# Optimization experiments

Hardware: AMD Instinct MI355X
Metric: run time of the kernel (lower is better)

The kernel has to match this reference:

```python
import jax, jax.numpy as jnp
import numpy as np

BETA = 0.9
ADAPT_RATE = 0.1


def _surrogate_spike(x):
    gate = jax.nn.sigmoid(5.0 * x)
    hard = (x > 0).astype(x.dtype)
    return jax.lax.stop_gradient(hard - gate) + gate


def setup_inputs() -> dict:
    key = jax.random.key(0)
    k1, k2, k3, k4, k5 = jax.random.split(key, 5)
    B, T, D, H = 64, 256, 512, 1024
    x = jax.random.normal(k1, (B, T, D), dtype=jnp.float32)
    # fc_in: Linear(D, H); fc_out: Linear(H, 1)
    W_in = jax.random.normal(k2, (H, D), dtype=jnp.float32) * (1.0 / np.sqrt(D))
    b_in = jax.random.normal(k3, (H,), dtype=jnp.float32) * 0.01
    W_out = jax.random.normal(k4, (1, H), dtype=jnp.float32) * (1.0 / np.sqrt(H))
    b_out = jax.random.normal(k5, (1,), dtype=jnp.float32) * 0.01
    return {"x": x, "W_in": W_in, "b_in": b_in, "W_out": W_out, "b_out": b_out}


def reference(x, W_in, b_in, W_out, b_out):
    B, T, D = x.shape
    H = W_in.shape[0]
    # batch fc_in over all timesteps outside the recurrence
    pre = jnp.einsum('btd,hd->bth', x, W_in) + b_in  # [B,T,H]

    def step(carry, p_t):
        mem, adapt = carry
        mem = BETA * mem + p_t - adapt
        spk = _surrogate_spike(mem)
        adapt = adapt + ADAPT_RATE * spk
        mem = mem - spk  # reset_mode == 'subtract'
        return (mem, adapt), spk

    init = (jnp.zeros((B, H), x.dtype), jnp.zeros((B, H), x.dtype))
    _, spks = jax.lax.scan(step, init, jnp.swapaxes(pre, 0, 1))  # spks: [T,B,H]

    # mean_t fc_out(spk_t) == fc_out(mean_t spk_t) since fc_out is affine
    spk_mean = spks.mean(axis=0)  # [B,H]
    return spk_mean @ W_out.T + b_out  # [B,1]
```

## Files before the change

kernel.cpp:

```cpp
#include <hip/hip_runtime.h>

constexpr int Bb = 64;
constexpr int Tt = 256;
constexpr int Dd = 512;
constexpr int Hh = 1024;
constexpr int Mm = Bb * Tt;

typedef _Float16 half8 __attribute__((ext_vector_type(8)));
typedef _Float16 half4v __attribute__((ext_vector_type(4)));
typedef float floatx16 __attribute__((ext_vector_type(16)));

#define GPTR(x) ((const __attribute__((address_space(1))) void*)(x))
#define LPTR(x) ((__attribute__((address_space(3))) void*)(x))

__global__ __launch_bounds__(256) void convert_t(const float* __restrict__ x,
                                                 const float* __restrict__ Win,
                                                 _Float16* __restrict__ xh,
                                                 _Float16* __restrict__ xl,
                                                 _Float16* __restrict__ wh,
                                                 _Float16* __restrict__ wl,
                                                 const float* __restrict__ bout,
                                                 float* __restrict__ out) {
    __shared__ _Float16 lh[64 * 72];
    __shared__ _Float16 ll[64 * 72];
    const int tid = threadIdx.x;
    const int k0 = blockIdx.x * 64;

    if (blockIdx.x == 0 && blockIdx.y == 0 && tid < Bb) out[tid] = bout[0];

    const float* src;
    _Float16 *dh, *dl;
    int nrows, m0;
    if (blockIdx.y < 256) {
        src = x; dh = xh; dl = xl; nrows = Mm; m0 = blockIdx.y * 64;
    } else {
        src = Win; dh = wh; dl = wl; nrows = Hh; m0 = (blockIdx.y - 256) * 64;
    }

#pragma unroll
    for (int i = 0; i < 4; ++i) {
        const int lin = tid + i * 256;
        const int row = lin >> 4;
        const int c4 = (lin & 15) * 4;
        const float4 v = *(const float4*)(src + (size_t)(m0 + row) * Dd + k0 + c4);
        const float va[4] = {v.x, v.y, v.z, v.w};
        half4v h, l;
#pragma unroll
        for (int q = 0; q < 4; ++q) {
            const _Float16 hi = (_Float16)va[q];
            h[q] = hi;
            l[q] = (_Float16)((va[q] - (float)hi) * 4096.0f);
        }
        *(half4v*)&lh[row * 72 + c4] = h;
        *(half4v*)&ll[row * 72 + c4] = l;
    }
    __syncthreads();
#pragma unroll
    for (int i = 0; i < 2; ++i) {
        const int lin = tid + i * 256;
        const int kc = lin >> 6;
        const int mm = lin & 63;
        const half8 h = *(const half8*)&lh[mm * 72 + kc * 8];
        const half8 l = *(const half8*)&ll[mm * 72 + kc * 8];
        const size_t g = (size_t)(k0 / 8 + kc) * nrows + m0 + mm;
        *(half8*)(dh + g * 8) = h;
        *(half8*)(dl + g * 8) = l;
    }
}

__global__ __launch_bounds__(256) void gemm_f16x2(const _Float16* __restrict__ xh,
                                                  const _Float16* __restrict__ xl,
                                                  const _Float16* __restrict__ wh,
                                                  const _Float16* __restrict__ wl,
                                                  const float* __restrict__ bin,
                                                  float* __restrict__ pre) {
    __shared__ _Float16 lds[2][4][4096];

    const int tid = threadIdx.x;
    const int id = blockIdx.x;
    const int j  = id & 7;
    const int s  = id >> 3;
    const int m0 = (((s >> 3) << 3) | j) * 128;
    const int n0 = (s & 7) * 128;

    const int lane = tid & 63;
    const int wave = tid >> 6;
    const int wm = (wave & 1) * 64;
    const int wn = (wave >> 1) * 64;
    const int lr = lane & 31;
    const int lk = lane >> 5;

    floatx16 acc[2][2], accx[2][2];
#pragma unroll
    for (int mi = 0; mi < 2; ++mi)
#pragma unroll
        for (int ni = 0; ni < 2; ++ni)
#pragma unroll
            for (int r = 0; r < 16; ++r) { acc[mi][ni][r] = 0.0f; accx[mi][ni][r] = 0.0f; }

#define STAGE(buf, kc0)                                                              \
    do {                                                                             \
        _Pragma("unroll")                                                            \
        for (int i_ = 0; i_ < 2; ++i_) {                                             \
            const int c_ = tid + i_ * 256;                                           \
            const int kp_ = c_ >> 7;                                                 \
            const int row_ = c_ & 127;                                               \
            const size_t ga_ = ((size_t)((kc0) + kp_) * Mm + m0 + row_) * 8;         \
            const size_t gb_ = ((size_t)((kc0) + kp_) * Hh + n0 + row_) * 8;         \
            __builtin_amdgcn_global_load_lds(GPTR(xh + ga_), LPTR(&lds[buf][0][c_ * 8]), 16, 0, 0); \
            __builtin_amdgcn_global_load_lds(GPTR(xl + ga_), LPTR(&lds[buf][1][c_ * 8]), 16, 0, 0); \
            __builtin_amdgcn_global_load_lds(GPTR(wh + gb_), LPTR(&lds[buf][2][c_ * 8]), 16, 0, 0); \
            __builtin_amdgcn_global_load_lds(GPTR(wl + gb_), LPTR(&lds[buf][3][c_ * 8]), 16, 0, 0); \
        }                                                                            \
    } while (0)

    STAGE(0, 0);

    for (int ss = 0; ss < 16; ++ss) {
        __syncthreads();
        if (ss < 15) STAGE((ss + 1) & 1, (ss + 1) * 4);
        const int cur = ss & 1;
#pragma unroll
        for (int s2 = 0; s2 < 2; ++s2) {
            half8 ah[2], al[2], bh[2], bl[2];
#pragma unroll
            for (int mi = 0; mi < 2; ++mi) {
                const int ci = (s2 * 2 + lk) * 128 + wm + mi * 32 + lr;
                ah[mi] = *(const half8*)&lds[cur][0][ci * 8];
                al[mi] = *(const half8*)&lds[cur][1][ci * 8];
            }
#pragma unroll
            for (int ni = 0; ni < 2; ++ni) {
                const int ci = (s2 * 2 + lk) * 128 + wn + ni * 32 + lr;
                bh[ni] = *(const half8*)&lds[cur][2][ci * 8];
                bl[ni] = *(const half8*)&lds[cur][3][ci * 8];
            }
#pragma unroll
            for (int mi = 0; mi < 2; ++mi)
#pragma unroll
                for (int ni = 0; ni < 2; ++ni) {
                    acc[mi][ni]  = __builtin_amdgcn_mfma_f32_32x32x16_f16(ah[mi], bh[ni], acc[mi][ni], 0, 0, 0);
                    accx[mi][ni] = __builtin_amdgcn_mfma_f32_32x32x16_f16(ah[mi], bl[ni], accx[mi][ni], 0, 0, 0);
                    accx[mi][ni] = __builtin_amdgcn_mfma_f32_32x32x16_f16(al[mi], bh[ni], accx[mi][ni], 0, 0, 0);
                }
        }
    }
#undef STAGE

    const float bv0 = bin[n0 + wn + lr];
    const float bv1 = bin[n0 + wn + 32 + lr];
#pragma unroll
    for (int mi = 0; mi < 2; ++mi)
#pragma unroll
        for (int ni = 0; ni < 2; ++ni) {
            const float bv = ni ? bv1 : bv0;
#pragma unroll
            for (int r = 0; r < 16; ++r) {
                const int row = (r & 3) + 8 * (r >> 2) + 4 * lk;
                const int m = m0 + wm + mi * 32 + row;
                const int n = n0 + wn + ni * 32 + lr;
                pre[(size_t)m * Hh + n] =
                    acc[mi][ni][r] + accx[mi][ni][r] * (1.0f / 4096.0f) + bv;
            }
        }
}

#define BK 16
#define BMP 132
__global__ __launch_bounds__(256) void gemm_pre(const float* __restrict__ x,
                                                const float* __restrict__ Win,
                                                const float* __restrict__ bin,
                                                float* __restrict__ pre) {
    __shared__ float As[BK][BMP];
    __shared__ float Bs[BK][BMP];
    const int tid = threadIdx.x;
    const int m0 = blockIdx.y * 128;
    const int n0 = blockIdx.x * 128;
    const int tx = tid & 15;
    const int ty = tid >> 4;
    float acc[8][8];
#pragma unroll
    for (int i = 0; i < 8; ++i)
#pragma unroll
        for (int jj = 0; jj < 8; ++jj) acc[i][jj] = 0.0f;
    const float* Aptr = x + (size_t)m0 * Dd;
    const float* Bptr = Win + (size_t)n0 * Dd;
    for (int k0 = 0; k0 < Dd; k0 += BK) {
#pragma unroll
        for (int i = 0; i < 2; ++i) {
            const int lin = tid + i * 256;
            const int row = lin >> 2;
            const int kq = (lin & 3) << 2;
            const float4 av = *(const float4*)(Aptr + (size_t)row * Dd + k0 + kq);
            const float4 bv = *(const float4*)(Bptr + (size_t)row * Dd + k0 + kq);
            As[kq + 0][row] = av.x; As[kq + 1][row] = av.y;
            As[kq + 2][row] = av.z; As[kq + 3][row] = av.w;
            Bs[kq + 0][row] = bv.x; Bs[kq + 1][row] = bv.y;
            Bs[kq + 2][row] = bv.z; Bs[kq + 3][row] = bv.w;
        }
        __syncthreads();
#pragma unroll
        for (int kk = 0; kk < BK; ++kk) {
            const float4 a0 = *(const float4*)&As[kk][ty * 4];
            const float4 a1 = *(const float4*)&As[kk][ty * 4 + 64];
            const float4 b0 = *(const float4*)&Bs[kk][tx * 4];
            const float4 b1 = *(const float4*)&Bs[kk][tx * 4 + 64];
            const float a[8] = {a0.x, a0.y, a0.z, a0.w, a1.x, a1.y, a1.z, a1.w};
            const float b[8] = {b0.x, b0.y, b0.z, b0.w, b1.x, b1.y, b1.z, b1.w};
#pragma unroll
            for (int i = 0; i < 8; ++i)
#pragma unroll
                for (int jj = 0; jj < 8; ++jj) acc[i][jj] += a[i] * b[jj];
        }
        __syncthreads();
    }
#pragma unroll
    for (int i = 0; i < 8; ++i) {
        const int m = m0 + ((i < 4) ? (ty * 4 + i) : (64 + ty * 4 + i - 4));
#pragma unroll
        for (int half = 0; half < 2; ++half) {
            const int n = n0 + tx * 4 + half * 64;
            float4 v;
            v.x = acc[i][half * 4 + 0] + bin[n + 0];
            v.y = acc[i][half * 4 + 1] + bin[n + 1];
            v.z = acc[i][half * 4 + 2] + bin[n + 2];
            v.w = acc[i][half * 4 + 3] + bin[n + 3];
            *(float4*)(pre + (size_t)m * Hh + n) = v;
        }
    }
}

__global__ __launch_bounds__(64) void init_out(const float* __restrict__ bout,
                                               float* __restrict__ out) {
    out[threadIdx.x] = bout[0];
}

__global__ __launch_bounds__(64) void alif_scan(const float* __restrict__ pre,
                                                const float* __restrict__ Wout,
                                                float* __restrict__ out) {
    const int h = blockIdx.x * 64 + threadIdx.x;
    const int b = blockIdx.y;
    const float* p = pre + (size_t)b * Tt * Hh + h;

    float buf[32];
#pragma unroll
    for (int jj = 0; jj < 32; ++jj) buf[jj] = p[(size_t)jj * Hh];

    float mem = 0.0f, adapt = 0.0f, cnt = 0.0f;
    for (int t0 = 0; t0 < Tt; t0 += 32) {
        float cur[32];
#pragma unroll
        for (int jj = 0; jj < 32; ++jj) cur[jj] = buf[jj];
        if (t0 + 32 < Tt) {
#pragma unroll
            for (int jj = 0; jj < 32; ++jj) buf[jj] = p[(size_t)(t0 + 32 + jj) * Hh];
        }
#pragma unroll
        for (int jj = 0; jj < 32; ++jj) {
            mem = 0.9f * mem + cur[jj] - adapt;
            const float spk = (mem > 0.0f) ? 1.0f : 0.0f;
            adapt += 0.1f * spk;
            mem -= spk;
            cnt += spk;
        }
    }

    float val = cnt * Wout[h] * (1.0f / (float)Tt);
#pragma unroll
    for (int off = 32; off > 0; off >>= 1) val += __shfl_down(val, off, 64);
    if (threadIdx.x == 0) atomicAdd(&out[b], val);
}

extern "C" void kernel_launch(void* const* d_in, const int* in_sizes, int n_in,
                              void* d_out, int out_size, void* d_ws, size_t ws_size,
                              hipStream_t stream) {
    const float* x    = (const float*)d_in[0];
    const float* Win  = (const float*)d_in[1];
    const float* bin  = (const float*)d_in[2];
    const float* Wout = (const float*)d_in[3];
    const float* bout = (const float*)d_in[4];
    float* out = (float*)d_out;

    const size_t pre_bytes = (size_t)Mm * Hh * 4;
    const size_t xh_bytes  = (size_t)Mm * Dd * 2;
    const size_t wh_bytes  = (size_t)Hh * Dd * 2;
    float* pre = (float*)d_ws;

    const size_t need = pre_bytes + 2 * xh_bytes + 2 * wh_bytes + 4096;
    if (ws_size >= need) {
        char* base = (char*)d_ws + pre_bytes;
        _Float16* xh = (_Float16*)base;
        _Float16* xl = (_Float16*)(base + xh_bytes);
        _Float16* wh = (_Float16*)(base + 2 * xh_bytes);
        _Float16* wl = (_Float16*)(base + 2 * xh_bytes + wh_bytes);

        convert_t<<<dim3(8, 272), 256, 0, stream>>>(x, Win, xh, xl, wh, wl, bout, out);

        gemm_f16x2<<<1024, 256, 0, stream>>>(xh, xl, wh, wl, bin, pre);

        alif_scan<<<dim3(Hh / 64, Bb), 64, 0, stream>>>(pre, Wout, out);
    } else {
        init_out<<<1, 64, 0, stream>>>(bout, out);
        dim3 g1(Hh / 128, Mm / 128);
        gemm_pre<<<g1, 256, 0, stream>>>(x, Win, bin, pre);
        alif_scan<<<dim3(Hh / 64, Bb), 64, 0, stream>>>(pre, Wout, out);
    }
}
```

Before: 152.0 us.

## Load W_in fragments directly from global into registers, bypassing LDS

The B operand (wh/wl) is no longer staged through shared memory. Each wave now loads its own fragments from global memory into registers, double-buffered one half-step ahead. This halves LDS footprint and LDS read traffic per step. In exchange the two waves sharing an n-range load the same W data redundantly, register pressure rises, and global loads sit on the MFMA critical path.

```diff
diff --git a/kernel.cpp b/kernel.cpp
--- a/kernel.cpp
+++ b/kernel.cpp
@@ -74,7 +74,7 @@
                                                   const _Float16* __restrict__ wl,
                                                   const float* __restrict__ bin,
                                                   float* __restrict__ pre) {
-    __shared__ _Float16 lds[2][4][4096];
+    __shared__ _Float16 lds[2][2][4096];
 
     const int tid = threadIdx.x;
     const int id = blockIdx.x;
@@ -98,7 +98,7 @@
 #pragma unroll
             for (int r = 0; r < 16; ++r) { acc[mi][ni][r] = 0.0f; accx[mi][ni][r] = 0.0f; }
 
-#define STAGE(buf, kc0)                                                              \
+#define STAGE_A(buf, kc0)                                                            \
     do {                                                                             \
         _Pragma("unroll")                                                            \
         for (int i_ = 0; i_ < 2; ++i_) {                                             \
@@ -106,23 +106,36 @@
             const int kp_ = c_ >> 7;                                                 \
             const int row_ = c_ & 127;                                               \
             const size_t ga_ = ((size_t)((kc0) + kp_) * Mm + m0 + row_) * 8;         \
-            const size_t gb_ = ((size_t)((kc0) + kp_) * Hh + n0 + row_) * 8;         \
             __builtin_amdgcn_global_load_lds(GPTR(xh + ga_), LPTR(&lds[buf][0][c_ * 8]), 16, 0, 0); \
             __builtin_amdgcn_global_load_lds(GPTR(xl + ga_), LPTR(&lds[buf][1][c_ * 8]), 16, 0, 0); \
-            __builtin_amdgcn_global_load_lds(GPTR(wh + gb_), LPTR(&lds[buf][2][c_ * 8]), 16, 0, 0); \
-            __builtin_amdgcn_global_load_lds(GPTR(wl + gb_), LPTR(&lds[buf][3][c_ * 8]), 16, 0, 0); \
         }                                                                            \
     } while (0)
 
-    STAGE(0, 0);
+    const size_t bbase = (size_t)(n0 + wn + lr) * 8;
+    half8 bset[2][4];
+#define LOAD_B(rot, hs)                                                              \
+    do {                                                                             \
+        const size_t off_ = (size_t)((hs) * 2 + lk) * (Hh * 8) + bbase;              \
+        bset[rot][0] = *(const half8*)(wh + off_);                                   \
+        bset[rot][1] = *(const half8*)(wh + off_ + 256);                             \
+        bset[rot][2] = *(const half8*)(wl + off_);                                   \
+        bset[rot][3] = *(const half8*)(wl + off_ + 256);                             \
+    } while (0)
+
+    STAGE_A(0, 0);
+    LOAD_B(0, 0);
 
     for (int ss = 0; ss < 16; ++ss) {
         __syncthreads();
-        if (ss < 15) STAGE((ss + 1) & 1, (ss + 1) * 4);
+        if (ss < 15) STAGE_A((ss + 1) & 1, (ss + 1) * 4);
         const int cur = ss & 1;
 #pragma unroll
         for (int s2 = 0; s2 < 2; ++s2) {
-            half8 ah[2], al[2], bh[2], bl[2];
+            const int hs = ss * 2 + s2;
+            const int rot = hs & 1;
+            if (hs < 31) LOAD_B(rot ^ 1, hs + 1);
+
+            half8 ah[2], al[2];
 #pragma unroll
             for (int mi = 0; mi < 2; ++mi) {
                 const int ci = (s2 * 2 + lk) * 128 + wm + mi * 32 + lr;
@@ -130,22 +143,17 @@
                 al[mi] = *(const half8*)&lds[cur][1][ci * 8];
             }
 #pragma unroll
-            for (int ni = 0; ni < 2; ++ni) {
-                const int ci = (s2 * 2 + lk) * 128 + wn + ni * 32 + lr;
-                bh[ni] = *(const half8*)&lds[cur][2][ci * 8];
-                bl[ni] = *(const half8*)&lds[cur][3][ci * 8];
-            }
-#pragma unroll
             for (int mi = 0; mi < 2; ++mi)
 #pragma unroll
                 for (int ni = 0; ni < 2; ++ni) {
-                    acc[mi][ni]  = __builtin_amdgcn_mfma_f32_32x32x16_f16(ah[mi], bh[ni], acc[mi][ni], 0, 0, 0);
-                    accx[mi][ni] = __builtin_amdgcn_mfma_f32_32x32x16_f16(ah[mi], bl[ni], accx[mi][ni], 0, 0, 0);
-                    accx[mi][ni] = __builtin_amdgcn_mfma_f32_32x32x16_f16(al[mi], bh[ni], accx[mi][ni], 0, 0, 0);
+                    acc[mi][ni]  = __builtin_amdgcn_mfma_f32_32x32x16_f16(ah[mi], bset[rot][ni],     acc[mi][ni], 0, 0, 0);
+                    accx[mi][ni] = __builtin_amdgcn_mfma_f32_32x32x16_f16(ah[mi], bset[rot][2 + ni], accx[mi][ni], 0, 0, 0);
+                    accx[mi][ni] = __builtin_amdgcn_mfma_f32_32x32x16_f16(al[mi], bset[rot][ni],     accx[mi][ni], 0, 0, 0);
                 }
         }
     }
-#undef STAGE
+#undef STAGE_A
+#undef LOAD_B
 
     const float bv0 = bin[n0 + wn + lr];
     const float bv1 = bin[n0 + wn + 32 + lr];
```

Result: no change. 152.6 us (+0.4%).

## Load GEMM operands directly from global into registers, dropping LDS staging

Applied to the files above, without the earlier changes.

The split-fp16 GEMM no longer stages A/B tiles through shared memory with global_load_lds and barriers. Each wave now loads its own MFMA fragments straight from global memory into a register double-buffer and prefetches the next k-step. Launch bounds also request two blocks per CU. This removes LDS traffic and __syncthreads, but every wave re-fetches data that other waves in the block share, which raises global and L2 traffic. The added register pressure may also hurt occupancy.

```diff
diff --git a/kernel.cpp b/kernel.cpp
--- a/kernel.cpp
+++ b/kernel.cpp
@@ -9,9 +9,6 @@
 typedef _Float16 half8 __attribute__((ext_vector_type(8)));
 typedef _Float16 half4v __attribute__((ext_vector_type(4)));
 typedef float floatx16 __attribute__((ext_vector_type(16)));
-
-#define GPTR(x) ((const __attribute__((address_space(1))) void*)(x))
-#define LPTR(x) ((__attribute__((address_space(3))) void*)(x))
 
 __global__ __launch_bounds__(256) void convert_t(const float* __restrict__ x,
                                                  const float* __restrict__ Win,
@@ -68,14 +65,12 @@
     }
 }
 
-__global__ __launch_bounds__(256) void gemm_f16x2(const _Float16* __restrict__ xh,
-                                                  const _Float16* __restrict__ xl,
-                                                  const _Float16* __restrict__ wh,
-                                                  const _Float16* __restrict__ wl,
-                                                  const float* __restrict__ bin,
-                                                  float* __restrict__ pre) {
-    __shared__ _Float16 lds[2][4][4096];
-
+__global__ __launch_bounds__(256, 2) void gemm_f16x2(const _Float16* __restrict__ xh,
+                                                     const _Float16* __restrict__ xl,
+                                                     const _Float16* __restrict__ wh,
+                                                     const _Float16* __restrict__ wl,
+                                                     const float* __restrict__ bin,
+                                                     float* __restrict__ pre) {
     const int tid = threadIdx.x;
     const int id = blockIdx.x;
     const int j  = id & 7;
@@ -98,54 +93,41 @@
 #pragma unroll
             for (int r = 0; r < 16; ++r) { acc[mi][ni][r] = 0.0f; accx[mi][ni][r] = 0.0f; }
 
-#define STAGE(buf, kc0)                                                              \
-    do {                                                                             \
-        _Pragma("unroll")                                                            \
-        for (int i_ = 0; i_ < 2; ++i_) {                                             \
-            const int c_ = tid + i_ * 256;                                           \
-            const int kp_ = c_ >> 7;                                                 \
-            const int row_ = c_ & 127;                                               \
-            const size_t ga_ = ((size_t)((kc0) + kp_) * Mm + m0 + row_) * 8;         \
-            const size_t gb_ = ((size_t)((kc0) + kp_) * Hh + n0 + row_) * 8;         \
-            __builtin_amdgcn_global_load_lds(GPTR(xh + ga_), LPTR(&lds[buf][0][c_ * 8]), 16, 0, 0); \
-            __builtin_amdgcn_global_load_lds(GPTR(xl + ga_), LPTR(&lds[buf][1][c_ * 8]), 16, 0, 0); \
-            __builtin_amdgcn_global_load_lds(GPTR(wh + gb_), LPTR(&lds[buf][2][c_ * 8]), 16, 0, 0); \
-            __builtin_amdgcn_global_load_lds(GPTR(wl + gb_), LPTR(&lds[buf][3][c_ * 8]), 16, 0, 0); \
-        }                                                                            \
+    const size_t arow0 = (size_t)(m0 + wm + lr);
+    const size_t brow0 = (size_t)(n0 + wn + lr);
+
+    half8 aset[2][4];
+    half8 bset[2][4];
+
+#define LOAD_AB(rot, hs)                                                        \
+    do {                                                                        \
+        const size_t kA = (size_t)((hs) * 2 + lk) * Mm;                         \
+        const size_t kB = (size_t)((hs) * 2 + lk) * Hh;                         \
+        aset[rot][0] = *(const half8*)(xh + (kA + arow0) * 8);                  \
+        aset[rot][1] = *(const half8*)(xh + (kA + arow0 + 32) * 8);             \
+        aset[rot][2] = *(const half8*)(xl + (kA + arow0) * 8);                  \
+        aset[rot][3] = *(const half8*)(xl + (kA + arow0 + 32) * 8);             \
+        bset[rot][0] = *(const half8*)(wh + (kB + brow0) * 8);                  \
+        bset[rot][1] = *(const half8*)(wh + (kB + brow0 + 32) * 8);             \
+        bset[rot][2] = *(const half8*)(wl + (kB + brow0) * 8);                  \
+        bset[rot][3] = *(const half8*)(wl + (kB + brow0 + 32) * 8);             \
     } while (0)
 
-    STAGE(0, 0);
-
-    for (int ss = 0; ss < 16; ++ss) {
-        __syncthreads();
-        if (ss < 15) STAGE((ss + 1) & 1, (ss + 1) * 4);
-        const int cur = ss & 1;
-#pragma unroll
-        for (int s2 = 0; s2 < 2; ++s2) {
-            half8 ah[2], al[2], bh[2], bl[2];
-#pragma unroll
-            for (int mi = 0; mi < 2; ++mi) {
-                const int ci = (s2 * 2 + lk) * 128 + wm + mi * 32 + lr;
-                ah[mi] = *(const half8*)&lds[cur][0][ci * 8];
-                al[mi] = *(const half8*)&lds[cur][1][ci * 8];
+    LOAD_AB(0, 0);
+
+    for (int hs = 0; hs < 32; ++hs) {
+        const int rot = hs & 1;
+        if (hs < 31) LOAD_AB(rot ^ 1, hs + 1);
+#pragma unroll
+        for (int mi = 0; mi < 2; ++mi)
+#pragma unroll
+            for (int ni = 0; ni < 2; ++ni) {
+                acc[mi][ni]  = __builtin_amdgcn_mfma_f32_32x32x16_f16(aset[rot][mi],     bset[rot][ni],     acc[mi][ni], 0, 0, 0);
+                accx[mi][ni] = __builtin_amdgcn_mfma_f32_32x32x16_f16(aset[rot][mi],     bset[rot][2 + ni], accx[mi][ni], 0, 0, 0);
+                accx[mi][ni] = __builtin_amdgcn_mfma_f32_32x32x16_f16(aset[rot][2 + mi], bset[rot][ni],     accx[mi][ni], 0, 0, 0);
             }
-#pragma unroll
-            for (int ni = 0; ni < 2; ++ni) {
-                const int ci = (s2 * 2 + lk) * 128 + wn + ni * 32 + lr;
-                bh[ni] = *(const half8*)&lds[cur][2][ci * 8];
-                bl[ni] = *(const half8*)&lds[cur][3][ci * 8];
-            }
-#pragma unroll
-            for (int mi = 0; mi < 2; ++mi)
-#pragma unroll
-                for (int ni = 0; ni < 2; ++ni) {
-                    acc[mi][ni]  = __builtin_amdgcn_mfma_f32_32x32x16_f16(ah[mi], bh[ni], acc[mi][ni], 0, 0, 0);
-                    accx[mi][ni] = __builtin_amdgcn_mfma_f32_32x32x16_f16(ah[mi], bl[ni], accx[mi][ni], 0, 0, 0);
-                    accx[mi][ni] = __builtin_amdgcn_mfma_f32_32x32x16_f16(al[mi], bh[ni], accx[mi][ni], 0, 0, 0);
-                }
-        }
-    }
-#undef STAGE
+    }
+#undef LOAD_AB
 
     const float bv0 = bin[n0 + wn + lr];
     const float bv1 = bin[n0 + wn + 32 + lr];
```

After: 158.3 us. 1.04x slower.
